# Optimization experiments

Hardware: AMD Instinct MI355X
Metric: run time of the kernel (lower is better)

## Reference

```python
import jax, jax.numpy as jnp
import numpy as np

B, D, T = 8, 1024, 2048          # batch, input_dim, time
CD, CS = 256, 8192               # codebook_dim, codebook_size


def _wn_weight(v, g):
    # torch weight_norm for Conv1d(k=1): weight = g * v / ||v|| with norm over
    # all dims except the output-channel dim. v: (out, in), g: (out, 1).
    return g * v / jnp.linalg.norm(v, axis=1, keepdims=True)


def setup_inputs() -> dict:
    key = jax.random.key(0)
    k0, k1, k2, k3 = jax.random.split(key, 4)
    z = jax.random.normal(k0, (B, D, T), dtype=jnp.float32)
    # in_proj: WNConv1d(input_dim -> codebook_dim, k=1)
    in_v = jax.random.normal(k1, (CD, D), dtype=jnp.float32) * 0.02
    in_g = jnp.ones((CD, 1), dtype=jnp.float32)
    in_b = jnp.zeros((CD,), dtype=jnp.float32)
    # out_proj: WNConv1d(codebook_dim -> input_dim, k=1)
    out_v = jax.random.normal(k2, (D, CD), dtype=jnp.float32) * 0.02
    out_g = jnp.ones((D, 1), dtype=jnp.float32)
    out_b = jnp.zeros((D,), dtype=jnp.float32)
    codebook = jax.random.normal(k3, (CS, CD), dtype=jnp.float32)
    return {"z": z, "in_v": in_v, "in_g": in_g, "in_b": in_b,
            "out_v": out_v, "out_g": out_g, "out_b": out_b,
            "codebook": codebook}


def reference(z, in_v, in_g, in_b, out_v, out_g, out_b, codebook):
    # in_proj (1x1 conv == per-timestep linear): (B, D, T) -> (B, CD, T)
    w_in = _wn_weight(in_v, in_g)
    z_e = jnp.einsum('bdt,cd->bct', z, w_in) + in_b[None, :, None]

    # flatten to (N, CD), N = B*T
    enc = z_e.transpose(0, 2, 1).reshape(-1, z_e.shape[1])

    # squared euclidean cdist via GEMM: ||e||^2 - 2 e.c^T + ||c||^2
    dist = (jnp.sum(enc * enc, axis=1, keepdims=True)
            - 2.0 * enc @ codebook.T
            + jnp.sum(codebook * codebook, axis=1)[None, :])  # (N, CS)

    indices = jnp.argmax(-dist, axis=1).reshape(z.shape[0], -1)  # (B, T)

    # decode_code: embedding gather then channels-first: (B, CD, T)
    z_q_code = codebook[indices].transpose(0, 2, 1)

    # out_proj: (B, CD, T) -> (B, D, T)
    w_out = _wn_weight(out_v, out_g)
    z_q = jnp.einsum('bct,dc->bdt', z_q_code, w_out) + out_b[None, :, None]
    return z_q, indices, z_e
```

## Files before the change

kernel.cpp:

```cpp
#include <hip/hip_runtime.h>
#include <math.h>

#define B_  8
#define D_  1024
#define T_  2048
#define CD_ 256
#define CS_ 8192
#define N_  (B_*T_)

#define NSPLIT 8
#define CODES_PER_SPLIT (CS_/NSPLIT)
#define NT_SPLIT (CODES_PER_SPLIT/64)
#define DELTA 1.5f

#define ROWS_PER_WAVE 64
#define SCAN_ROWS 256
#define TILE_CODES 64

#define WS_ZEN   0
#define WS_CBB   2097152
#define WS_WH    (WS_CBB + 1048576)
#define WS_WM    (WS_WH + 131072)
#define WS_WOB   (WS_WM + 131072)
#define WS_C2    (WS_WOB + 131072)
#define WS_CNT   (WS_C2 + CS_)
#define WS_CAND  (WS_CNT + N_)
#define WS_IDX   (WS_CAND + N_*16)

#define OUT_ZQ  0
#define OUT_IDX (B_*D_*T_)
#define OUT_ZE  (OUT_IDX + B_*T_)

using short8v = __attribute__((ext_vector_type(8))) short;
using float4v = __attribute__((ext_vector_type(4))) float;

__device__ __forceinline__ float wave_sum64(float v) {
#pragma unroll
  for (int off = 32; off >= 1; off >>= 1) v += __shfl_xor(v, off);
  return v;
}

__device__ __forceinline__ unsigned short f2bf_rne(float f) {
  unsigned int u = __float_as_uint(f);
  u += 0x7fffu + ((u >> 16) & 1u);
  return (unsigned short)(u >> 16);
}

__device__ __forceinline__ float bf2f(unsigned short u) {
  return __uint_as_float(((unsigned)u) << 16);
}

__device__ __forceinline__ void gload_lds16(const void* g, void* l) {
  __builtin_amdgcn_global_load_lds(
      (const __attribute__((address_space(1))) void*)g,
      (__attribute__((address_space(3))) void*)l, 16, 0, 0);
}

__global__ __launch_bounds__(256) void prep_all(
    const float* __restrict__ in_v, const float* __restrict__ in_g,
    const float* __restrict__ out_v, const float* __restrict__ out_g,
    const float* __restrict__ cb,
    unsigned short* __restrict__ wh, unsigned short* __restrict__ wm,
    unsigned short* __restrict__ wob,
    float* __restrict__ c2, unsigned short* __restrict__ cbb) {
  __shared__ float sh[4];
  int blk = blockIdx.x, tid = threadIdx.x;
  if (blk < CD_) {
    int c = blk;
    float v[4]; float s = 0.f;
#pragma unroll
    for (int i = 0; i < 4; ++i) {
      v[i] = in_v[c * D_ + tid + 256 * i];
      s = fmaf(v[i], v[i], s);
    }
    s = wave_sum64(s);
    if ((tid & 63) == 0) sh[tid >> 6] = s;
    __syncthreads();
    float tot = sh[0] + sh[1] + sh[2] + sh[3];
    float scale = in_g[c] / sqrtf(tot);
#pragma unroll
    for (int i = 0; i < 4; ++i) {
      int d = tid + 256 * i;
      float x = v[i] * scale;
      unsigned short h = f2bf_rne(x);
      float r1 = x - bf2f(h);
      unsigned short m = (unsigned short)(__float_as_uint(r1) >> 16);
      wh[c * D_ + d] = h; wm[c * D_ + d] = m;
    }
  } else if (blk < CD_ + D_) {
    int d = blk - CD_;
    float v = out_v[d * CD_ + tid];
    float s = wave_sum64(v * v);
    if ((tid & 63) == 0) sh[tid >> 6] = s;
    __syncthreads();
    float tot = sh[0] + sh[1] + sh[2] + sh[3];
    float scale = out_g[d] / sqrtf(tot);
    wob[d * CD_ + tid] = f2bf_rne(v * scale);
  } else {
    size_t i = (size_t)(blk - CD_ - D_) * 256 + tid;
    float4 v0 = *(const float4*)&cb[i * 8];
    float4 v1 = *(const float4*)&cb[i * 8 + 4];
    float f[8] = {v0.x, v0.y, v0.z, v0.w, v1.x, v1.y, v1.z, v1.w};
    unsigned short us[8];
    float sq = 0.f;
#pragma unroll
    for (int m = 0; m < 8; ++m) {
      us[m] = f2bf_rne(f[m]);
      sq = fmaf(f[m], f[m], sq);
    }
    *(uint4*)&cbb[i * 8] = *(uint4*)&us[0];
#pragma unroll
    for (int off = 1; off < 32; off <<= 1) sq += __shfl_xor(sq, off);
    if ((tid & 31) == 0) c2[i >> 5] = sq;
  }
}

__global__ __launch_bounds__(256, 2) void ze_mfma(
    const float* __restrict__ z,
    const unsigned short* __restrict__ whp, const unsigned short* __restrict__ wmp,
    const float* __restrict__ in_b,
    float* __restrict__ out, unsigned short* __restrict__ zeN) {
  __shared__ __align__(16) char zbuf[2][16 * 1040];
  __shared__ __align__(16) unsigned short abuf[2][2][2048];
  int tid = threadIdx.x;
  int w = tid >> 6, l = tid & 63;
  int lrow = l & 15, lg = l >> 4;
  int t0 = blockIdx.x * 128, c0 = blockIdx.y * 64, b = blockIdx.z;
  const float* zb = z + (size_t)b * D_ * T_;
  char* zbuf_b = &zbuf[0][0];
  char* abuf_b = (char*)&abuf[0][0][0];

  auto stage = [&](int buf, int kc) {
#pragma unroll
    for (int i = 0; i < 4; ++i) {
      int g = w * 4 + i;
      int row = 2 * g + (l >> 5);
      gload_lds16(&zb[(size_t)(kc + row) * T_ + t0 + (l & 31) * 4],
                  zbuf_b + buf * 16640 + g * 1040);
    }
    int c = w * 16 + (l >> 2);
    int doff = (l & 3) * 8;
    gload_lds16(&whp[(size_t)(c0 + c) * D_ + kc + doff],
                abuf_b + buf * 8192 + w * 1024);
    gload_lds16(&wmp[(size_t)(c0 + c) * D_ + kc + doff],
                abuf_b + buf * 8192 + 4096 + w * 1024);
  };

  float4v acc[4][2];
#pragma unroll
  for (int rf = 0; rf < 4; ++rf)
#pragma unroll
    for (int cf = 0; cf < 2; ++cf) acc[rf][cf] = (float4v){0.f, 0.f, 0.f, 0.f};

  stage(0, 0);
  int cur = 0;
  for (int kt = 0; kt < D_ / 32; ++kt) {
    if (kt + 1 < D_ / 32) {
      stage(cur ^ 1, (kt + 1) * 32);
      asm volatile("s_waitcnt vmcnt(6)" ::: "memory");
    } else {
      asm volatile("s_waitcnt vmcnt(0)" ::: "memory");
    }
    __builtin_amdgcn_sched_barrier(0);
    __builtin_amdgcn_s_barrier();

    short8v bh[2], bm[2];
#pragma unroll
    for (int cf = 0; cf < 2; ++cf) {
      const char* zp = zbuf_b + cur * 16640 + lg * 4160 +
                       (w * 32 + cf * 16 + lrow) * 4;
      float x[8];
#pragma unroll
      for (int j = 0; j < 8; ++j)
        x[j] = *(const float*)(zp + (j >> 1) * 1040 + (j & 1) * 512);
      __align__(16) unsigned short h8[8], m8[8];
#pragma unroll
      for (int j = 0; j < 8; ++j) {
        unsigned short h = f2bf_rne(x[j]);
        float r1 = x[j] - bf2f(h);
        m8[j] = (unsigned short)(__float_as_uint(r1) >> 16);
        h8[j] = h;
      }
      bh[cf] = *(const short8v*)h8;
      bm[cf] = *(const short8v*)m8;
    }
    short8v ah[4], am[4];
#pragma unroll
    for (int rf = 0; rf < 4; ++rf) {
      int coff = (rf * 16 + lrow) * 64 + lg * 16;
      const char* ab = abuf_b + cur * 8192 + coff;
      ah[rf] = *(const short8v*)(ab);
      am[rf] = *(const short8v*)(ab + 4096);
    }
#pragma unroll
    for (int rf = 0; rf < 4; ++rf)
#pragma unroll
      for (int cf = 0; cf < 2; ++cf) {
        float4v a_ = acc[rf][cf];
        a_ = __builtin_amdgcn_mfma_f32_16x16x32_bf16(ah[rf], bh[cf], a_, 0, 0, 0);
        a_ = __builtin_amdgcn_mfma_f32_16x16x32_bf16(am[rf], bh[cf], a_, 0, 0, 0);
        a_ = __builtin_amdgcn_mfma_f32_16x16x32_bf16(ah[rf], bm[cf], a_, 0, 0, 0);
        a_ = __builtin_amdgcn_mfma_f32_16x16x32_bf16(am[rf], bm[cf], a_, 0, 0, 0);
        acc[rf][cf] = a_;
      }
    __builtin_amdgcn_s_barrier();
    cur ^= 1;
  }

  int tbase = t0 + w * 32;
#pragma unroll
  for (int rf = 0; rf < 4; ++rf) {
    float bv[4];
#pragma unroll
    for (int rg = 0; rg < 4; ++rg) bv[rg] = in_b[c0 + rf * 16 + lg * 4 + rg];
#pragma unroll
    for (int cf = 0; cf < 2; ++cf) {
      int t = tbase + cf * 16 + lrow;
#pragma unroll
      for (int rg = 0; rg < 4; ++rg) {
        int c = c0 + rf * 16 + lg * 4 + rg;
        out[OUT_ZE + (size_t)(b * CD_ + c) * T_ + t] = acc[rf][cf][rg] + bv[rg];
      }
      __align__(8) unsigned short us[4];
#pragma unroll
      for (int rg = 0; rg < 4; ++rg) us[rg] = f2bf_rne(acc[rf][cf][rg] + bv[rg]);
      *(uint2*)&zeN[(size_t)(b * T_ + t) * CD_ + c0 + rf * 16 + lg * 4] =
          *(uint2*)us;
    }
  }
}

template <int COLLECT>
__global__ __launch_bounds__(256, 2) void vq_scan(
    const unsigned short* __restrict__ zeN, const unsigned short* __restrict__ cbb,
    const float* __restrict__ c2, float* __restrict__ bestq,
    int* __restrict__ cnt, int* __restrict__ cand) {
  __shared__ __align__(16) unsigned short smem[2][TILE_CODES * CD_];
  int tid = threadIdx.x;
  int w = tid >> 6, l = tid & 63;
  int lrow = l & 15, lg = l >> 4;
  int rowbase = blockIdx.x * SCAN_ROWS + w * ROWS_PER_WAVE;
  int cq = blockIdx.y;
  int cbase0 = cq * CODES_PER_SPLIT;

  if (COLLECT == 0 && cq == 0)
    cnt[blockIdx.x * SCAN_ROWS + tid] = 0;

  short8v a[4][8];
#pragma unroll
  for (int rf = 0; rf < 4; ++rf)
#pragma unroll
    for (int ks = 0; ks < 8; ++ks)
      a[rf][ks] = *(const short8v*)&zeN[((size_t)(rowbase + rf * 16 + lrow)) * CD_ + ks * 32 + lg * 8];

  float best[16];
  float thr[16];
#pragma unroll
  for (int s = 0; s < 16; ++s) best[s] = -3.4e38f;
  if (COLLECT) {
#pragma unroll
    for (int s = 0; s < 16; ++s) {
      int rf = s >> 2, rg = s & 3;
      thr[s] = bestq[rowbase + rf * 16 + lg * 4 + rg];
    }
  }

  int lhalf = l >> 5;
  int lcol = (l & 31) * 16;
  char* smem_b = (char*)&smem[0][0];
  const char* cbb_b = (const char*)cbb;
  int xsw = (lrow & 7) << 4;

  auto stage = [&](int buf, int cbase) {
#pragma unroll
    for (int r = 0; r < 8; ++r) {
      int code = w * 16 + r * 2 + lhalf;
      size_t goff = (size_t)(cbase + code) * 512 + (size_t)(lcol ^ ((code & 7) << 4));
      gload_lds16(cbb_b + goff, smem_b + buf * 32768 + (w * 8 + r) * 1024);
    }
  };

  stage(0, cbase0);

  for (int t = 0; t < NT_SPLIT; ++t) {
    int buf = t & 1;
    int cbase = cbase0 + t * TILE_CODES;

    float hc2[4];
#pragma unroll
    for (int cf = 0; cf < 4; ++cf) hc2[cf] = 0.5f * c2[cbase + cf * 16 + lrow];

    if (t + 1 < NT_SPLIT) {
      stage(buf ^ 1, cbase + TILE_CODES);
      asm volatile("s_waitcnt vmcnt(8)" ::: "memory");
    } else {
      asm volatile("s_waitcnt vmcnt(0)" ::: "memory");
    }
    __builtin_amdgcn_sched_barrier(0);
    __builtin_amdgcn_s_barrier();

    const char* bufb = smem_b + buf * 32768;
#pragma unroll
    for (int cf = 0; cf < 4; ++cf) {
      const char* bbase = bufb + (cf * 16 + lrow) * 512;
      float4v acc[4];
#pragma unroll
      for (int rf = 0; rf < 4; ++rf) acc[rf] = (float4v){0.f, 0.f, 0.f, 0.f};
#pragma unroll
      for (int ks = 0; ks < 8; ++ks) {
        short8v bfrag = *(const short8v*)(bbase + ((ks * 64 + lg * 16) ^ xsw));
        acc[0] = __builtin_amdgcn_mfma_f32_16x16x32_bf16(a[0][ks], bfrag, acc[0], 0, 0, 0);
        acc[1] = __builtin_amdgcn_mfma_f32_16x16x32_bf16(a[1][ks], bfrag, acc[1], 0, 0, 0);
        acc[2] = __builtin_amdgcn_mfma_f32_16x16x32_bf16(a[2][ks], bfrag, acc[2], 0, 0, 0);
        acc[3] = __builtin_amdgcn_mfma_f32_16x16x32_bf16(a[3][ks], bfrag, acc[3], 0, 0, 0);
      }
      int ci = cbase + cf * 16 + lrow;
#pragma unroll
      for (int rf = 0; rf < 4; ++rf)
#pragma unroll
        for (int rg = 0; rg < 4; ++rg) {
          float sc = acc[rf][rg] - hc2[cf];
          int slot = rf * 4 + rg;
          if (COLLECT) {
            if (sc >= thr[slot]) {
              int row = rowbase + rf * 16 + lg * 4 + rg;
              int pos = atomicAdd(&cnt[row], 1);
              if (pos < 16) cand[row * 16 + pos] = ci;
            }
          } else {
            best[slot] = fmaxf(best[slot], sc);
          }
        }
    }
    __builtin_amdgcn_s_barrier();
  }

  if (!COLLECT) {
#pragma unroll
    for (int s = 0; s < 16; ++s) {
      float v = best[s];
#pragma unroll
      for (int off = 1; off < 16; off <<= 1) v = fmaxf(v, __shfl_xor(v, off));
      best[s] = v;
    }
    if (lrow == 0) {
#pragma unroll
      for (int s = 0; s < 16; ++s) {
        int rf = s >> 2, rg = s & 3;
        bestq[cq * N_ + rowbase + rf * 16 + lg * 4 + rg] = best[s];
      }
    }
  }
}

__global__ __launch_bounds__(256) void vq_rowthr(float* __restrict__ bestq) {
  int n = blockIdx.x * 256 + threadIdx.x;
  float m = bestq[n];
#pragma unroll
  for (int q = 1; q < NSPLIT; ++q) m = fmaxf(m, bestq[q * N_ + n]);
  bestq[n] = m - DELTA;
}

__global__ __launch_bounds__(256) void vq_rescore(
    const float* __restrict__ ze, const float* __restrict__ cb,
    const int* __restrict__ cnt, const int* __restrict__ cand,
    float* __restrict__ out, int* __restrict__ idx_ws) {
  int tid = threadIdx.x;
  int n = blockIdx.x * 64 + (tid >> 2);
  int j = tid & 3;
  int b = n >> 11, t = n & (T_ - 1);
  const float* zr = ze + ((size_t)b * CD_) * T_ + t;
  int m = cnt[n]; if (m > 16) m = 16;
  float bd = 3.4e38f; int bi = 0x7fffffff;
  for (int i = 0; i < m; ++i) {
    int c = cand[n * 16 + i];
    const float* cr = cb + (size_t)c * CD_;
    float d = 0.f;
    for (int k = j; k < CD_; k += 4) {
      float diff = zr[(size_t)k * T_] - cr[k];
      d = fmaf(diff, diff, d);
    }
    d += __shfl_xor(d, 1);
    d += __shfl_xor(d, 2);
    if (d < bd || (d == bd && c < bi)) { bd = d; bi = c; }
  }
  if (j == 0) {
    idx_ws[n] = bi;
    out[OUT_IDX + n] = (float)bi;
  }
}

__global__ __launch_bounds__(256, 2) void zq_mfma(
    const unsigned short* __restrict__ wob, const unsigned short* __restrict__ cbb,
    const float* __restrict__ out_bias, const int* __restrict__ idx,
    float* __restrict__ out) {
  __shared__ __align__(16) unsigned short Bs[64 * CD_];
  __shared__ int idxs[64];
  int tid = threadIdx.x;
  int w = tid >> 6, l = tid & 63;
  int lrow = l & 15, lg = l >> 4;
  int t0 = blockIdx.x * 64, d0 = blockIdx.y * 256, b = blockIdx.z;
  int rowbase = d0 + w * 64;

  if (tid < 64) idxs[tid] = idx[b * T_ + t0 + tid];

  short8v a[4][8];
#pragma unroll
  for (int rf = 0; rf < 4; ++rf)
#pragma unroll
    for (int ks = 0; ks < 8; ++ks)
      a[rf][ks] = *(const short8v*)&wob[((size_t)(rowbase + rf * 16 + lrow)) * CD_ + ks * 32 + lg * 8];

  __syncthreads();

  int lhalf = l >> 5;
  int lcol = (l & 31) * 16;
  char* Bs_b = (char*)&Bs[0];
  const char* cbb_b = (const char*)cbb;
#pragma unroll
  for (int r = 0; r < 8; ++r) {
    int t = w * 16 + r * 2 + lhalf;
    int row = idxs[t];
    size_t goff = (size_t)row * 512 + (size_t)(lcol ^ ((t & 7) << 4));
    gload_lds16(cbb_b + goff, Bs_b + (w * 8 + r) * 1024);
  }
  __syncthreads();

  int xsw = (lrow & 7) << 4;
  float4v acc[4][4];
#pragma unroll
  for (int rf = 0; rf < 4; ++rf)
#pragma unroll
    for (int cf = 0; cf < 4; ++cf) acc[rf][cf] = (float4v){0.f, 0.f, 0.f, 0.f};
#pragma unroll
  for (int cf = 0; cf < 4; ++cf) {
    const char* bbase = Bs_b + (cf * 16 + lrow) * 512;
#pragma unroll
    for (int ks = 0; ks < 8; ++ks) {
      short8v bfrag = *(const short8v*)(bbase + ((ks * 64 + lg * 16) ^ xsw));
      acc[0][cf] = __builtin_amdgcn_mfma_f32_16x16x32_bf16(a[0][ks], bfrag, acc[0][cf], 0, 0, 0);
      acc[1][cf] = __builtin_amdgcn_mfma_f32_16x16x32_bf16(a[1][ks], bfrag, acc[1][cf], 0, 0, 0);
      acc[2][cf] = __builtin_amdgcn_mfma_f32_16x16x32_bf16(a[2][ks], bfrag, acc[2][cf], 0, 0, 0);
      acc[3][cf] = __builtin_amdgcn_mfma_f32_16x16x32_bf16(a[3][ks], bfrag, acc[3][cf], 0, 0, 0);
    }
  }
#pragma unroll
  for (int rf = 0; rf < 4; ++rf) {
    float bias[4];
#pragma unroll
    for (int rg = 0; rg < 4; ++rg) bias[rg] = out_bias[rowbase + rf * 16 + lg * 4 + rg];
#pragma unroll
    for (int cf = 0; cf < 4; ++cf) {
      int t = t0 + cf * 16 + lrow;
#pragma unroll
      for (int rg = 0; rg < 4; ++rg) {
        int d = rowbase + rf * 16 + lg * 4 + rg;
        out[OUT_ZQ + (size_t)(b * D_ + d) * T_ + t] = acc[rf][cf][rg] + bias[rg];
      }
    }
  }
}

extern "C" void kernel_launch(void* const* d_in, const int* in_sizes, int n_in,
                              void* d_out, int out_size, void* d_ws,
                              size_t ws_size, hipStream_t stream) {
  const float* z     = (const float*)d_in[0];
  const float* in_v  = (const float*)d_in[1];
  const float* in_g  = (const float*)d_in[2];
  const float* in_b  = (const float*)d_in[3];
  const float* out_v = (const float*)d_in[4];
  const float* out_g = (const float*)d_in[5];
  const float* out_b = (const float*)d_in[6];
  const float* cb    = (const float*)d_in[7];
  float* out = (float*)d_out;
  float* ws  = (float*)d_ws;

  unsigned short* zeN = (unsigned short*)(ws + WS_ZEN);
  unsigned short* cbb = (unsigned short*)(ws + WS_CBB);
  unsigned short* wh  = (unsigned short*)(ws + WS_WH);
  unsigned short* wm  = (unsigned short*)(ws + WS_WM);
  unsigned short* wob = (unsigned short*)(ws + WS_WOB);
  float* c2     = ws + WS_C2;
  int*   cnt    = (int*)(ws + WS_CNT);
  int*   cand   = (int*)(ws + WS_CAND);
  int*   idxw   = (int*)(ws + WS_IDX);
  float* bestq  = out + OUT_ZQ;

  prep_all<<<CD_ + D_ + CS_ * CD_ / 8 / 256, 256, 0, stream>>>(
      in_v, in_g, out_v, out_g, cb, wh, wm, wob, c2, cbb);

  ze_mfma<<<dim3(T_ / 128, CD_ / 64, B_), 256, 0, stream>>>(
      z, wh, wm, in_b, out, zeN);

  vq_scan<0><<<dim3(N_ / SCAN_ROWS, NSPLIT), 256, 0, stream>>>(
      zeN, cbb, c2, bestq, cnt, cand);
  vq_rowthr<<<N_ / 256, 256, 0, stream>>>(bestq);
  vq_scan<1><<<dim3(N_ / SCAN_ROWS, NSPLIT), 256, 0, stream>>>(
      zeN, cbb, c2, bestq, cnt, cand);
  vq_rescore<<<N_ / 64, 256, 0, stream>>>(out + OUT_ZE, cb, cnt, cand, out, idxw);

  zq_mfma<<<dim3(T_ / 64, D_ / 256, B_), 256, 0, stream>>>(wob, cbb, out_b, idxw, out);
}
```

Before: 313.6 us.

## Switch VQ distance scan to FP8 MFMA with wider rescoring margin

The encoder output and a new FP8 copy of the codebook are packed into FP8, and both scan passes use fp8 16x16x32 MFMA instead of bf16. This halves the LDS and global traffic per codebook tile and doubles the MFMA rate. To cover the larger FP8 approximation error, the candidate margin grows from 1.5 to 7.5 and the candidate cap from 16 to 48. Exact selection still happens in the fp32 rescore, so that pass gets more expensive, and rows with more than 48 candidates could return a wrong index.

Result: slower. 548.7 us (+75.0%).

```diff
diff --git a/kernel.cpp b/kernel.cpp
--- a/kernel.cpp
+++ b/kernel.cpp
@@ -11,21 +11,23 @@
 #define NSPLIT 8
 #define CODES_PER_SPLIT (CS_/NSPLIT)
 #define NT_SPLIT (CODES_PER_SPLIT/64)
-#define DELTA 1.5f
+#define DELTA 7.5f
+#define CAP 48
 
 #define ROWS_PER_WAVE 64
 #define SCAN_ROWS 256
 #define TILE_CODES 64
 
-#define WS_ZEN   0
-#define WS_CBB   2097152
-#define WS_WH    (WS_CBB + 1048576)
-#define WS_WM    (WS_WH + 131072)
-#define WS_WOB   (WS_WM + 131072)
-#define WS_C2    (WS_WOB + 131072)
-#define WS_CNT   (WS_C2 + CS_)
-#define WS_CAND  (WS_CNT + N_)
-#define WS_IDX   (WS_CAND + N_*16)
+#define WS_ZEN8  0
+#define WS_CBB   1048576
+#define WS_CBB8  2097152
+#define WS_WH    2621440
+#define WS_WM    2752512
+#define WS_WOB   2883584
+#define WS_C2    3014656
+#define WS_CNT   3022848
+#define WS_CAND  3039232
+#define WS_IDX   3825664
 
 #define OUT_ZQ  0
 #define OUT_IDX (B_*D_*T_)
@@ -54,6 +56,12 @@
   __builtin_amdgcn_global_load_lds(
       (const __attribute__((address_space(1))) void*)g,
       (__attribute__((address_space(3))) void*)l, 16, 0, 0);
+}
+
+__device__ __forceinline__ int pack_fp8x4(float a, float b, float c, float d) {
+  int p = __builtin_amdgcn_cvt_pk_fp8_f32(a, b, 0, false);
+  p = __builtin_amdgcn_cvt_pk_fp8_f32(c, d, p, true);
+  return p;
 }
 
 __global__ __launch_bounds__(256) void prep_all(
@@ -62,7 +70,8 @@
     const float* __restrict__ cb,
     unsigned short* __restrict__ wh, unsigned short* __restrict__ wm,
     unsigned short* __restrict__ wob,
-    float* __restrict__ c2, unsigned short* __restrict__ cbb) {
+    float* __restrict__ c2, unsigned short* __restrict__ cbb,
+    unsigned char* __restrict__ cbb8) {
   __shared__ float sh[4];
   int blk = blockIdx.x, tid = threadIdx.x;
   if (blk < CD_) {
@@ -109,6 +118,10 @@
       sq = fmaf(f[m], f[m], sq);
     }
     *(uint4*)&cbb[i * 8] = *(uint4*)&us[0];
+    uint2 p8;
+    p8.x = (unsigned)pack_fp8x4(f[0], f[1], f[2], f[3]);
+    p8.y = (unsigned)pack_fp8x4(f[4], f[5], f[6], f[7]);
+    *(uint2*)&cbb8[i * 8] = p8;
 #pragma unroll
     for (int off = 1; off < 32; off <<= 1) sq += __shfl_xor(sq, off);
     if ((tid & 31) == 0) c2[i >> 5] = sq;
@@ -119,7 +132,7 @@
     const float* __restrict__ z,
     const unsigned short* __restrict__ whp, const unsigned short* __restrict__ wmp,
     const float* __restrict__ in_b,
-    float* __restrict__ out, unsigned short* __restrict__ zeN) {
+    float* __restrict__ out, unsigned char* __restrict__ zeN8) {
   __shared__ __align__(16) char zbuf[2][16 * 1040];
   __shared__ __align__(16) unsigned short abuf[2][2][2048];
   int tid = threadIdx.x;
@@ -216,26 +229,25 @@
 #pragma unroll
     for (int cf = 0; cf < 2; ++cf) {
       int t = tbase + cf * 16 + lrow;
+      float o[4];
 #pragma unroll
       for (int rg = 0; rg < 4; ++rg) {
+        o[rg] = acc[rf][cf][rg] + bv[rg];
         int c = c0 + rf * 16 + lg * 4 + rg;
-        out[OUT_ZE + (size_t)(b * CD_ + c) * T_ + t] = acc[rf][cf][rg] + bv[rg];
+        out[OUT_ZE + (size_t)(b * CD_ + c) * T_ + t] = o[rg];
       }
-      __align__(8) unsigned short us[4];
-#pragma unroll
-      for (int rg = 0; rg < 4; ++rg) us[rg] = f2bf_rne(acc[rf][cf][rg] + bv[rg]);
-      *(uint2*)&zeN[(size_t)(b * T_ + t) * CD_ + c0 + rf * 16 + lg * 4] =
-          *(uint2*)us;
+      int p = pack_fp8x4(o[0], o[1], o[2], o[3]);
+      *(int*)&zeN8[(size_t)(b * T_ + t) * CD_ + c0 + rf * 16 + lg * 4] = p;
     }
   }
 }
 
 template <int COLLECT>
 __global__ __launch_bounds__(256, 2) void vq_scan(
-    const unsigned short* __restrict__ zeN, const unsigned short* __restrict__ cbb,
+    const unsigned char* __restrict__ zeN8, const unsigned char* __restrict__ cbb8,
     const float* __restrict__ c2, float* __restrict__ bestq,
     int* __restrict__ cnt, int* __restrict__ cand) {
-  __shared__ __align__(16) unsigned short smem[2][TILE_CODES * CD_];
+  __shared__ __align__(16) unsigned char smem[2][TILE_CODES * 256];
   int tid = threadIdx.x;
   int w = tid >> 6, l = tid & 63;
   int lrow = l & 15, lg = l >> 4;
@@ -246,12 +258,12 @@
   if (COLLECT == 0 && cq == 0)
     cnt[blockIdx.x * SCAN_ROWS + tid] = 0;
 
-  short8v a[4][8];
+  long a[4][8];
 #pragma unroll
   for (int rf = 0; rf < 4; ++rf)
 #pragma unroll
     for (int ks = 0; ks < 8; ++ks)
-      a[rf][ks] = *(const short8v*)&zeN[((size_t)(rowbase + rf * 16 + lrow)) * CD_ + ks * 32 + lg * 8];
+      a[rf][ks] = *(const long*)&zeN8[((size_t)(rowbase + rf * 16 + lrow)) * 256 + ks * 32 + lg * 8];
 
   float best[16];
   float thr[16];
@@ -265,18 +277,18 @@
     }
   }
 
-  int lhalf = l >> 5;
-  int lcol = (l & 31) * 16;
-  char* smem_b = (char*)&smem[0][0];
-  const char* cbb_b = (const char*)cbb;
+  unsigned char* smem_b = &smem[0][0];
+  const unsigned char* cbb_b = cbb8;
   int xsw = (lrow & 7) << 4;
 
   auto stage = [&](int buf, int cbase) {
 #pragma unroll
-    for (int r = 0; r < 8; ++r) {
-      int code = w * 16 + r * 2 + lhalf;
-      size_t goff = (size_t)(cbase + code) * 512 + (size_t)(lcol ^ ((code & 7) << 4));
-      gload_lds16(cbb_b + goff, smem_b + buf * 32768 + (w * 8 + r) * 1024);
+    for (int r = 0; r < 4; ++r) {
+      int g = w * 4 + r;
+      int code = g * 4 + (l >> 4);
+      int base = (l & 15) * 16;
+      gload_lds16(cbb_b + (size_t)(cbase + code) * 256 + (base ^ ((code & 7) << 4)),
+                  smem_b + buf * 16384 + g * 1024 + (l & 15) * 16);
     }
   };
 
@@ -299,20 +311,20 @@
     __builtin_amdgcn_sched_barrier(0);
     __builtin_amdgcn_s_barrier();
 
-    const char* bufb = smem_b + buf * 32768;
+    const unsigned char* bufb = smem_b + buf * 16384;
 #pragma unroll
     for (int cf = 0; cf < 4; ++cf) {
-      const char* bbase = bufb + (cf * 16 + lrow) * 512;
+      const unsigned char* bbase = bufb + (cf * 16 + lrow) * 256;
       float4v acc[4];
 #pragma unroll
       for (int rf = 0; rf < 4; ++rf) acc[rf] = (float4v){0.f, 0.f, 0.f, 0.f};
 #pragma unroll
       for (int ks = 0; ks < 8; ++ks) {
-        short8v bfrag = *(const short8v*)(bbase + ((ks * 64 + lg * 16) ^ xsw));
-        acc[0] = __builtin_amdgcn_mfma_f32_16x16x32_bf16(a[0][ks], bfrag, acc[0], 0, 0, 0);
-        acc[1] = __builtin_amdgcn_mfma_f32_16x16x32_bf16(a[1][ks], bfrag, acc[1], 0, 0, 0);
-        acc[2] = __builtin_amdgcn_mfma_f32_16x16x32_bf16(a[2][ks], bfrag, acc[2], 0, 0, 0);
-        acc[3] = __builtin_amdgcn_mfma_f32_16x16x32_bf16(a[3][ks], bfrag, acc[3], 0, 0, 0);
+        long bfrag = *(const long*)(bbase + ((ks * 32 + lg * 8) ^ xsw));
+        acc[0] = __builtin_amdgcn_mfma_f32_16x16x32_fp8_fp8(a[0][ks], bfrag, acc[0], 0, 0, 0);
+        acc[1] = __builtin_amdgcn_mfma_f32_16x16x32_fp8_fp8(a[1][ks], bfrag, acc[1], 0, 0, 0);
+        acc[2] = __builtin_amdgcn_mfma_f32_16x16x32_fp8_fp8(a[2][ks], bfrag, acc[2], 0, 0, 0);
+        acc[3] = __builtin_amdgcn_mfma_f32_16x16x32_fp8_fp8(a[3][ks], bfrag, acc[3], 0, 0, 0);
       }
       int ci = cbase + cf * 16 + lrow;
 #pragma unroll
@@ -325,7 +337,7 @@
             if (sc >= thr[slot]) {
               int row = rowbase + rf * 16 + lg * 4 + rg;
               int pos = atomicAdd(&cnt[row], 1);
-              if (pos < 16) cand[row * 16 + pos] = ci;
+              if (pos < CAP) cand[row * CAP + pos] = ci;
             }
           } else {
             best[slot] = fmaxf(best[slot], sc);
@@ -370,10 +382,10 @@
   int j = tid & 3;
   int b = n >> 11, t = n & (T_ - 1);
   const float* zr = ze + ((size_t)b * CD_) * T_ + t;
-  int m = cnt[n]; if (m > 16) m = 16;
+  int m = cnt[n]; if (m > CAP) m = CAP;
   float bd = 3.4e38f; int bi = 0x7fffffff;
   for (int i = 0; i < m; ++i) {
-    int c = cand[n * 16 + i];
+    int c = cand[n * CAP + i];
     const float* cr = cb + (size_t)c * CD_;
     float d = 0.f;
     for (int k = j; k < CD_; k += 4) {
@@ -475,8 +487,9 @@
   float* out = (float*)d_out;
   float* ws  = (float*)d_ws;
 
-  unsigned short* zeN = (unsigned short*)(ws + WS_ZEN);
+  unsigned char* zeN8 = (unsigned char*)(ws + WS_ZEN8);
   unsigned short* cbb = (unsigned short*)(ws + WS_CBB);
+  unsigned char* cbb8 = (unsigned char*)(ws + WS_CBB8);
   unsigned short* wh  = (unsigned short*)(ws + WS_WH);
   unsigned short* wm  = (unsigned short*)(ws + WS_WM);
   unsigned short* wob = (unsigned short*)(ws + WS_WOB);
@@ -487,16 +500,16 @@
   float* bestq  = out + OUT_ZQ;
 
   prep_all<<<CD_ + D_ + CS_ * CD_ / 8 / 256, 256, 0, stream>>>(
-      in_v, in_g, out_v, out_g, cb, wh, wm, wob, c2, cbb);
+      in_v, in_g, out_v, out_g, cb, wh, wm, wob, c2, cbb, cbb8);
 
   ze_mfma<<<dim3(T_ / 128, CD_ / 64, B_), 256, 0, stream>>>(
-      z, wh, wm, in_b, out, zeN);
+      z, wh, wm, in_b, out, zeN8);
 
   vq_scan<0><<<dim3(N_ / SCAN_ROWS, NSPLIT), 256, 0, stream>>>(
-      zeN, cbb, c2, bestq, cnt, cand);
+      zeN8, cbb8, c2, bestq, cnt, cand);
   vq_rowthr<<<N_ / 256, 256, 0, stream>>>(bestq);
   vq_scan<1><<<dim3(N_ / SCAN_ROWS, NSPLIT), 256, 0, stream>>>(
-      zeN, cbb, c2, bestq, cnt, cand);
+      zeN8, cbb8, c2, bestq, cnt, cand);
   vq_rescore<<<N_ / 64, 256, 0, stream>>>(out + OUT_ZE, cb, cnt, cand, out, idxw);
 
   zq_mfma<<<dim3(T_ / 64, D_ / 256, B_), 256, 0, stream>>>(wob, cbb, out_b, idxw, out);
```
